# Kernel tuning notes

Measured on AMD Instinct MI355X. Metric: run time of the kernel, lower is better.

The kernel has to match this reference:

```python
import jax, jax.numpy as jnp
import numpy as np

B, T, C, H, O = 64, 256, 2048, 512, 11
THRESHOLD = 1.0
LEAK = 0.003
OUTPUT_LEAK = LEAK * 0.5


def setup_inputs() -> dict:
    key = jax.random.key(0)
    k1, k2, k3, k4 = jax.random.split(key, 4)
    x = jax.random.normal(k1, (B, T, C), dtype=jnp.float32)
    # xavier_uniform(gain=0.1) for fc1: bound = 0.1*sqrt(6/(C+H))
    b1 = 0.1 * np.sqrt(6.0 / (C + H))
    w1 = jax.random.uniform(k2, (H, C), jnp.float32, -b1, b1)
    # orthogonal(gain=0.1) for fc_rec -> approximate with small gaussian scaled like orthogonal rows
    w_rec = 0.1 * jnp.linalg.qr(jax.random.normal(k3, (H, H), jnp.float32))[0]
    b2 = 0.3 * np.sqrt(6.0 / (H + O))
    w2 = jax.random.uniform(k4, (O, H), jnp.float32, -b2, b2)
    return {"x": x, "w1": w1, "w_rec": w_rec, "w2": w2}


def reference(x, w1, w_rec, w2):
    batch, t_steps, _ = x.shape
    n_hidden = w1.shape[0]
    n_output = w2.shape[0]
    dt = x.dtype

    def step(carry, x_t):
        v1, spk1, v2, out_sum = carry
        # input + recurrent current: [B,H]
        i1 = x_t @ w1.T + spk1 @ w_rec.T
        # subtractive LIF: leak, threshold, subtractive reset
        v1 = v1 + i1 - LEAK
        spk = (v1 >= THRESHOLD).astype(dt)
        v1 = v1 - spk * THRESHOLD
        # non-spiking output accumulator neuron: [B,O]
        i2 = spk @ w2.T
        v2 = jnp.maximum(v2 + i2 - OUTPUT_LEAK, 0.0)
        out_sum = out_sum + v2
        return (v1, spk, v2, out_sum), None

    init = (
        jnp.zeros((batch, n_hidden), dt),
        jnp.zeros((batch, n_hidden), dt),
        jnp.zeros((batch, n_output), dt),
        jnp.zeros((batch, n_output), dt),
    )
    (_, _, _, out_sum), _ = jax.lax.scan(step, init, jnp.swapaxes(x, 0, 1))
    return out_sum / t_steps
```

## Files before the change

kernel.cpp:

```cpp
#include <hip/hip_runtime.h>
#include <cstddef>

#define B_ 64
#define T_ 256
#define C_ 2048
#define H_ 512
#define O_ 11
#define THRESH 1.0f
#define LEAK_ 0.003f
#define OLEAK_ 0.0015f

typedef float v2f __attribute__((ext_vector_type(2)));

__global__ __launch_bounds__(256) void transpose_wrec(const float* __restrict__ w,
                                                      float* __restrict__ wt) {
    __shared__ float tile[32][33];
    int tx = threadIdx.x, ty = threadIdx.y;
    int x = blockIdx.x * 32 + tx;
    int y = blockIdx.y * 32 + ty;
#pragma unroll
    for (int i = 0; i < 32; i += 8)
        tile[ty + i][tx] = w[(size_t)(y + i) * H_ + x];
    __syncthreads();
    int x2 = blockIdx.y * 32 + tx;
    int y2 = blockIdx.x * 32 + ty;
#pragma unroll
    for (int i = 0; i < 32; i += 8)
        wt[(size_t)(y2 + i) * H_ + x2] = tile[tx][ty + i];
}

#define BM 256
#define BN 128
#define BK 16

template <int S>
__global__ __launch_bounds__(256, 2) void gemm_ff(const float* __restrict__ A,
                                                  const float* __restrict__ Bw,
                                                  float* __restrict__ Pout) {
    const int K = C_;
    const int N = H_;
    const int kLen  = C_ / S;
    const int kBase = blockIdx.z * kLen;

    __shared__ float As[BK][BM + 4];
    __shared__ float Bs[BK][BN + 4];

    const int t  = threadIdx.x;
    const int tx = t & 15;
    const int ty = t >> 4;
    const int lr = t >> 2;
    const int lc = (t & 3) * 4;

    const float* Aptr = A  + (size_t)(blockIdx.y * BM + lr) * K + kBase + lc;
    const float* Bptr = Bw + (size_t)(blockIdx.x * BN + lr) * K + kBase + lc;

    v2f acc[16][4];
#pragma unroll
    for (int i = 0; i < 16; ++i)
#pragma unroll
        for (int j = 0; j < 4; ++j) acc[i][j] = (v2f){0.f, 0.f};

    for (int k0 = 0; k0 < kLen; k0 += BK) {
        float4 a0 = *(const float4*)(Aptr);
        float4 a1 = *(const float4*)(Aptr + (size_t)64  * K);
        float4 a2 = *(const float4*)(Aptr + (size_t)128 * K);
        float4 a3 = *(const float4*)(Aptr + (size_t)192 * K);
        float4 b0 = *(const float4*)(Bptr);
        float4 b1 = *(const float4*)(Bptr + (size_t)64 * K);
        Aptr += BK; Bptr += BK;

        __syncthreads();
        As[lc + 0][lr]       = a0.x; As[lc + 1][lr]       = a0.y;
        As[lc + 2][lr]       = a0.z; As[lc + 3][lr]       = a0.w;
        As[lc + 0][lr + 64]  = a1.x; As[lc + 1][lr + 64]  = a1.y;
        As[lc + 2][lr + 64]  = a1.z; As[lc + 3][lr + 64]  = a1.w;
        As[lc + 0][lr + 128] = a2.x; As[lc + 1][lr + 128] = a2.y;
        As[lc + 2][lr + 128] = a2.z; As[lc + 3][lr + 128] = a2.w;
        As[lc + 0][lr + 192] = a3.x; As[lc + 1][lr + 192] = a3.y;
        As[lc + 2][lr + 192] = a3.z; As[lc + 3][lr + 192] = a3.w;
        Bs[lc + 0][lr]       = b0.x; Bs[lc + 1][lr]       = b0.y;
        Bs[lc + 2][lr]       = b0.z; Bs[lc + 3][lr]       = b0.w;
        Bs[lc + 0][lr + 64]  = b1.x; Bs[lc + 1][lr + 64]  = b1.y;
        Bs[lc + 2][lr + 64]  = b1.z; Bs[lc + 3][lr + 64]  = b1.w;
        __syncthreads();

#pragma unroll
        for (int k = 0; k < BK; ++k) {
            float4 af0 = *(const float4*)&As[k][ty * 8];
            float4 af1 = *(const float4*)&As[k][ty * 8 + 4];
            float4 af2 = *(const float4*)&As[k][128 + ty * 8];
            float4 af3 = *(const float4*)&As[k][128 + ty * 8 + 4];
            float4 blo = *(const float4*)&Bs[k][tx * 4];
            float4 bhi = *(const float4*)&Bs[k][64 + tx * 4];
            v2f b0v = {blo.x, blo.y}, b1v = {blo.z, blo.w};
            v2f b2v = {bhi.x, bhi.y}, b3v = {bhi.z, bhi.w};
            float av[16] = {af0.x, af0.y, af0.z, af0.w, af1.x, af1.y, af1.z, af1.w,
                            af2.x, af2.y, af2.z, af2.w, af3.x, af3.y, af3.z, af3.w};
#pragma unroll
            for (int i = 0; i < 16; ++i) {
                v2f ai = {av[i], av[i]};
                acc[i][0] += ai * b0v;
                acc[i][1] += ai * b1v;
                acc[i][2] += ai * b2v;
                acc[i][3] += ai * b3v;
            }
        }
    }

    float* P = Pout + (size_t)blockIdx.z * ((size_t)B_ * T_ * H_);
#pragma unroll
    for (int i = 0; i < 16; ++i) {
        int row = blockIdx.y * BM + (i < 8 ? ty * 8 + i : 128 + ty * 8 + (i - 8));
        float* Cp = P + (size_t)row * N + blockIdx.x * BN;
        float4 c0 = {acc[i][0].x, acc[i][0].y, acc[i][1].x, acc[i][1].y};
        float4 c1 = {acc[i][2].x, acc[i][2].y, acc[i][3].x, acc[i][3].y};
        *(float4*)(Cp + tx * 4)      = c0;
        *(float4*)(Cp + 64 + tx * 4) = c1;
    }
}

template <int S>
__global__ __launch_bounds__(256) void reduce_parts(float* __restrict__ P) {
    const size_t n = (size_t)B_ * T_ * H_;
    size_t i = ((size_t)blockIdx.x * 256 + threadIdx.x) * 4;
    if (i >= n) return;
    float4 a = *(float4*)(P + i);
#pragma unroll
    for (int s = 1; s < S; ++s) {
        float4 bq = *(const float4*)(P + (size_t)s * n + i);
        a.x += bq.x; a.y += bq.y; a.z += bq.z; a.w += bq.w;
    }
    *(float4*)(P + i) = a;
}

__global__ __launch_bounds__(64) void snn_rec(const float* __restrict__ I1,
                                              const float* __restrict__ wrT,
                                              const float* __restrict__ w2,
                                              float* __restrict__ out) {
    const int b = blockIdx.x;
    const int L = threadIdx.x;

    const float* i1p = I1 + (size_t)b * T_ * H_ + L;
    const float* wrL = wrT + L;
    const float* w2L = w2 + (size_t)(L < O_ ? L : 0) * H_;

    float v1[8], pf[8];
    unsigned long long masks[8];
#pragma unroll
    for (int r = 0; r < 8; ++r) { v1[r] = 0.f; masks[r] = 0ull; pf[r] = i1p[r * 64]; }
    float v2 = 0.f, osum = 0.f;

    for (int t = 0; t < T_; ++t) {
        float acc[8];
#pragma unroll
        for (int r = 0; r < 8; ++r) acc[r] = pf[r] - LEAK_;

        const float* nx = i1p + (size_t)((t + 1 < T_) ? t + 1 : t) * H_;
#pragma unroll
        for (int r = 0; r < 8; ++r) pf[r] = nx[r * 64];

#pragma unroll
        for (int r2 = 0; r2 < 8; ++r2) {
            unsigned long long m = masks[r2];
            while (m) {
                int j = (r2 << 6) + __builtin_ctzll(m);
                m &= (m - 1);
                const float* wj = wrL + (size_t)j * H_;
#pragma unroll
                for (int r = 0; r < 8; ++r) acc[r] += wj[r * 64];
            }
        }

#pragma unroll
        for (int r = 0; r < 8; ++r) v1[r] += acc[r];
#pragma unroll
        for (int r = 0; r < 8; ++r) {
            masks[r] = __ballot(v1[r] >= THRESH);
            if (v1[r] >= THRESH) v1[r] -= THRESH;
        }

        float s = 0.f;
        if (L < O_) {
#pragma unroll
            for (int r2 = 0; r2 < 8; ++r2) {
                unsigned long long m = masks[r2];
                while (m) {
                    int j = (r2 << 6) + __builtin_ctzll(m);
                    m &= (m - 1);
                    s += w2L[j];
                }
            }
        }
        v2 = v2 + s - OLEAK_;
        v2 = v2 > 0.f ? v2 : 0.f;
        osum += v2;
    }
    if (L < O_) out[b * O_ + L] = osum * (1.0f / (float)T_);
}

extern "C" void kernel_launch(void* const* d_in, const int* in_sizes, int n_in,
                              void* d_out, int out_size, void* d_ws, size_t ws_size,
                              hipStream_t stream) {
    const float* x     = (const float*)d_in[0];
    const float* w1    = (const float*)d_in[1];
    const float* w_rec = (const float*)d_in[2];
    const float* w2    = (const float*)d_in[3];
    float* out = (float*)d_out;

    const size_t PART = (size_t)B_ * T_ * H_ * sizeof(float);
    const size_t WRT  = (size_t)H_ * H_ * sizeof(float);

    int S = 1;
    if (ws_size >= 4 * PART + WRT) S = 4;
    else if (ws_size >= 2 * PART + WRT) S = 2;

    float* P   = (float*)d_ws;
    float* wrT = (float*)((char*)d_ws + (size_t)S * PART);

    transpose_wrec<<<dim3(H_ / 32, H_ / 32), dim3(32, 8), 0, stream>>>(w_rec, wrT);

    dim3 ggrid(H_ / BN, (B_ * T_) / BM, S);
    const int rblocks = (int)(((size_t)B_ * T_ * H_ / 4 + 255) / 256);
    switch (S) {
        case 4:
            gemm_ff<4><<<ggrid, dim3(256), 0, stream>>>(x, w1, P);
            reduce_parts<4><<<dim3(rblocks), dim3(256), 0, stream>>>(P);
            break;
        case 2:
            gemm_ff<2><<<ggrid, dim3(256), 0, stream>>>(x, w1, P);
            reduce_parts<2><<<dim3(rblocks), dim3(256), 0, stream>>>(P);
            break;
        default:
            gemm_ff<1><<<ggrid, dim3(256), 0, stream>>>(x, w1, P);
            break;
    }
    snn_rec<<<dim3(B_), dim3(64), 0, stream>>>(P, wrT, w2, out);
}
```

Baseline: 777.5 us.

## Prefetch GEMM tiles in registers and restructure recurrent spike loop with batched gathers

The feedforward GEMM now uses 128x128 tiles with 128 threads and loads the next K-slice into registers while the current tile is computed, overlapping global loads with FMA work. The recurrent kernel builds a compact spike index list in shared memory each step and gathers recurrent weight rows in batches of eight, so loads can be issued in parallel instead of serially per spike. The output-neuron accumulation moves out of the time loop: spike masks are stored in shared memory and the output currents are computed in parallel after the loop. The trade-offs are more registers in the GEMM, more shared memory, and some redundant clamped loads in the gather.

Result: slower. 894.4 us (+15.0%).

```diff
diff --git a/kernel.cpp b/kernel.cpp
--- a/kernel.cpp
+++ b/kernel.cpp
@@ -29,12 +29,12 @@
         wt[(size_t)(y2 + i) * H_ + x2] = tile[tx][ty + i];
 }
 
-#define BM 256
+#define BM 128
 #define BN 128
 #define BK 16
 
 template <int S>
-__global__ __launch_bounds__(256, 2) void gemm_ff(const float* __restrict__ A,
+__global__ __launch_bounds__(128, 2) void gemm_ff(const float* __restrict__ A,
                                                   const float* __restrict__ Bw,
                                                   float* __restrict__ Pout) {
     const int K = C_;
@@ -51,8 +51,16 @@
     const int lr = t >> 2;
     const int lc = (t & 3) * 4;
 
-    const float* Aptr = A  + (size_t)(blockIdx.y * BM + lr) * K + kBase + lc;
-    const float* Bptr = Bw + (size_t)(blockIdx.x * BN + lr) * K + kBase + lc;
+    const float* Ap = A  + (size_t)(blockIdx.y * BM + lr) * K + kBase + lc;
+    const float* Bp = Bw + (size_t)(blockIdx.x * BN + lr) * K + kBase + lc;
+
+    float4 ar[4], br[4];
+#pragma unroll
+    for (int q = 0; q < 4; ++q) {
+        ar[q] = *(const float4*)(Ap + (size_t)(q * 32) * K);
+        br[q] = *(const float4*)(Bp + (size_t)(q * 32) * K);
+    }
+    Ap += BK; Bp += BK;
 
     v2f acc[16][4];
 #pragma unroll
@@ -60,42 +68,39 @@
 #pragma unroll
         for (int j = 0; j < 4; ++j) acc[i][j] = (v2f){0.f, 0.f};
 
-    for (int k0 = 0; k0 < kLen; k0 += BK) {
-        float4 a0 = *(const float4*)(Aptr);
-        float4 a1 = *(const float4*)(Aptr + (size_t)64  * K);
-        float4 a2 = *(const float4*)(Aptr + (size_t)128 * K);
-        float4 a3 = *(const float4*)(Aptr + (size_t)192 * K);
-        float4 b0 = *(const float4*)(Bptr);
-        float4 b1 = *(const float4*)(Bptr + (size_t)64 * K);
-        Aptr += BK; Bptr += BK;
-
+    const int nT = kLen / BK;
+    for (int kt = 0; kt < nT; ++kt) {
         __syncthreads();
-        As[lc + 0][lr]       = a0.x; As[lc + 1][lr]       = a0.y;
-        As[lc + 2][lr]       = a0.z; As[lc + 3][lr]       = a0.w;
-        As[lc + 0][lr + 64]  = a1.x; As[lc + 1][lr + 64]  = a1.y;
-        As[lc + 2][lr + 64]  = a1.z; As[lc + 3][lr + 64]  = a1.w;
-        As[lc + 0][lr + 128] = a2.x; As[lc + 1][lr + 128] = a2.y;
-        As[lc + 2][lr + 128] = a2.z; As[lc + 3][lr + 128] = a2.w;
-        As[lc + 0][lr + 192] = a3.x; As[lc + 1][lr + 192] = a3.y;
-        As[lc + 2][lr + 192] = a3.z; As[lc + 3][lr + 192] = a3.w;
-        Bs[lc + 0][lr]       = b0.x; Bs[lc + 1][lr]       = b0.y;
-        Bs[lc + 2][lr]       = b0.z; Bs[lc + 3][lr]       = b0.w;
-        Bs[lc + 0][lr + 64]  = b1.x; Bs[lc + 1][lr + 64]  = b1.y;
-        Bs[lc + 2][lr + 64]  = b1.z; Bs[lc + 3][lr + 64]  = b1.w;
+#pragma unroll
+        for (int q = 0; q < 4; ++q) {
+            As[lc + 0][lr + q * 32] = ar[q].x; As[lc + 1][lr + q * 32] = ar[q].y;
+            As[lc + 2][lr + q * 32] = ar[q].z; As[lc + 3][lr + q * 32] = ar[q].w;
+            Bs[lc + 0][lr + q * 32] = br[q].x; Bs[lc + 1][lr + q * 32] = br[q].y;
+            Bs[lc + 2][lr + q * 32] = br[q].z; Bs[lc + 3][lr + q * 32] = br[q].w;
+        }
         __syncthreads();
 
+        if (kt + 1 < nT) {
+#pragma unroll
+            for (int q = 0; q < 4; ++q) {
+                ar[q] = *(const float4*)(Ap + (size_t)(q * 32) * K);
+                br[q] = *(const float4*)(Bp + (size_t)(q * 32) * K);
+            }
+            Ap += BK; Bp += BK;
+        }
+
 #pragma unroll
         for (int k = 0; k < BK; ++k) {
-            float4 af0 = *(const float4*)&As[k][ty * 8];
-            float4 af1 = *(const float4*)&As[k][ty * 8 + 4];
-            float4 af2 = *(const float4*)&As[k][128 + ty * 8];
-            float4 af3 = *(const float4*)&As[k][128 + ty * 8 + 4];
-            float4 blo = *(const float4*)&Bs[k][tx * 4];
-            float4 bhi = *(const float4*)&Bs[k][64 + tx * 4];
-            v2f b0v = {blo.x, blo.y}, b1v = {blo.z, blo.w};
-            v2f b2v = {bhi.x, bhi.y}, b3v = {bhi.z, bhi.w};
-            float av[16] = {af0.x, af0.y, af0.z, af0.w, af1.x, af1.y, af1.z, af1.w,
-                            af2.x, af2.y, af2.z, af2.w, af3.x, af3.y, af3.z, af3.w};
+            float4 a0 = *(const float4*)&As[k][ty * 8];
+            float4 a1 = *(const float4*)&As[k][ty * 8 + 4];
+            float4 a2 = *(const float4*)&As[k][64 + ty * 8];
+            float4 a3 = *(const float4*)&As[k][64 + ty * 8 + 4];
+            float4 bq0 = *(const float4*)&Bs[k][tx * 4];
+            float4 bq1 = *(const float4*)&Bs[k][64 + tx * 4];
+            v2f b0v = {bq0.x, bq0.y}, b1v = {bq0.z, bq0.w};
+            v2f b2v = {bq1.x, bq1.y}, b3v = {bq1.z, bq1.w};
+            float av[16] = {a0.x, a0.y, a0.z, a0.w, a1.x, a1.y, a1.z, a1.w,
+                            a2.x, a2.y, a2.z, a2.w, a3.x, a3.y, a3.z, a3.w};
 #pragma unroll
             for (int i = 0; i < 16; ++i) {
                 v2f ai = {av[i], av[i]};
@@ -110,7 +115,7 @@
     float* P = Pout + (size_t)blockIdx.z * ((size_t)B_ * T_ * H_);
 #pragma unroll
     for (int i = 0; i < 16; ++i) {
-        int row = blockIdx.y * BM + (i < 8 ? ty * 8 + i : 128 + ty * 8 + (i - 8));
+        int row = blockIdx.y * BM + (i < 8 ? ty * 8 + i : 64 + ty * 8 + (i - 8));
         float* Cp = P + (size_t)row * N + blockIdx.x * BN;
         float4 c0 = {acc[i][0].x, acc[i][0].y, acc[i][1].x, acc[i][1].y};
         float4 c1 = {acc[i][2].x, acc[i][2].y, acc[i][3].x, acc[i][3].y};
@@ -140,62 +145,124 @@
     const int b = blockIdx.x;
     const int L = threadIdx.x;
 
+    __shared__ int                smask_lo[T_ * 8];
+    __shared__ int                smask_hi[T_ * 8];
+    __shared__ int                slist[2][H_];
+    __shared__ float              w2t[H_ * 12];
+    __shared__ float              i2s[T_ * 12];
+
     const float* i1p = I1 + (size_t)b * T_ * H_ + L;
-    const float* wrL = wrT + L;
-    const float* w2L = w2 + (size_t)(L < O_ ? L : 0) * H_;
 
     float v1[8], pf[8];
-    unsigned long long masks[8];
-#pragma unroll
-    for (int r = 0; r < 8; ++r) { v1[r] = 0.f; masks[r] = 0ull; pf[r] = i1p[r * 64]; }
-    float v2 = 0.f, osum = 0.f;
+#pragma unroll
+    for (int r = 0; r < 8; ++r) { v1[r] = 0.f; pf[r] = i1p[r * 64]; }
+
+    const unsigned long long below = (L == 0) ? 0ull : ((~0ull) >> (64 - L));
+    int pcnt = 0;
 
     for (int t = 0; t < T_; ++t) {
-        float acc[8];
-#pragma unroll
-        for (int r = 0; r < 8; ++r) acc[r] = pf[r] - LEAK_;
+        const int pb = t & 1;
+        const int prev = pb ^ 1;
+
+        float racc[8];
+#pragma unroll
+        for (int r = 0; r < 8; ++r) racc[r] = pf[r] - LEAK_;
+
+        for (int base = 0; base < pcnt; base += 8) {
+            int jj[8];
+#pragma unroll
+            for (int s = 0; s < 8; ++s) {
+                int ii = base + s;
+                if (ii > pcnt - 1) ii = pcnt - 1;
+                jj[s] = slist[prev][ii];
+            }
+            float vv[8][8];
+#pragma unroll
+            for (int s = 0; s < 8; ++s) {
+                const float* wj = wrT + (size_t)jj[s] * H_ + L;
+#pragma unroll
+                for (int r = 0; r < 8; ++r) vv[s][r] = wj[r * 64];
+            }
+#pragma unroll
+            for (int s = 0; s < 8; ++s) {
+                if (base + s < pcnt) {
+#pragma unroll
+                    for (int r = 0; r < 8; ++r) racc[r] += vv[s][r];
+                }
+            }
+        }
+
+        unsigned long long mk[8];
+#pragma unroll
+        for (int r = 0; r < 8; ++r) {
+            v1[r] += racc[r];
+            bool sp = (v1[r] >= THRESH);
+            mk[r] = __ballot(sp);
+            if (sp) v1[r] -= THRESH;
+        }
+
+        if (L == 0) {
+#pragma unroll
+            for (int r = 0; r < 8; ++r) {
+                smask_lo[t * 8 + r] = (int)(mk[r] & 0xffffffffull);
+                smask_hi[t * 8 + r] = (int)(mk[r] >> 32);
+            }
+        }
+
+        int cb = 0;
+#pragma unroll
+        for (int r = 0; r < 8; ++r) {
+            int pos = (int)__popcll(mk[r] & below);
+            if ((mk[r] >> L) & 1ull) slist[pb][cb + pos] = (r << 6) + L;
+            cb += (int)__popcll(mk[r]);
+        }
+        pcnt = cb;
 
         const float* nx = i1p + (size_t)((t + 1 < T_) ? t + 1 : t) * H_;
 #pragma unroll
         for (int r = 0; r < 8; ++r) pf[r] = nx[r * 64];
-
-#pragma unroll
-        for (int r2 = 0; r2 < 8; ++r2) {
-            unsigned long long m = masks[r2];
+    }
+
+    __syncthreads();
+
+    for (int j = L; j < H_; j += 64) {
+#pragma unroll
+        for (int o = 0; o < O_; ++o) w2t[j * 12 + o] = w2[o * H_ + j];
+    }
+    __syncthreads();
+
+    for (int tt = L; tt < T_; tt += 64) {
+        float s0 = 0.f, s1 = 0.f, s2 = 0.f, s3 = 0.f, s4 = 0.f, s5 = 0.f,
+              s6 = 0.f, s7 = 0.f, s8 = 0.f, s9 = 0.f, s10 = 0.f;
+#pragma unroll
+        for (int r = 0; r < 8; ++r) {
+            unsigned long long m =
+                ((unsigned long long)(unsigned)smask_lo[tt * 8 + r]) |
+                (((unsigned long long)(unsigned)smask_hi[tt * 8 + r]) << 32);
             while (m) {
-                int j = (r2 << 6) + __builtin_ctzll(m);
-                m &= (m - 1);
-                const float* wj = wrL + (size_t)j * H_;
-#pragma unroll
-                for (int r = 0; r < 8; ++r) acc[r] += wj[r * 64];
-            }
-        }
-
-#pragma unroll
-        for (int r = 0; r < 8; ++r) v1[r] += acc[r];
-#pragma unroll
-        for (int r = 0; r < 8; ++r) {
-            masks[r] = __ballot(v1[r] >= THRESH);
-            if (v1[r] >= THRESH) v1[r] -= THRESH;
-        }
-
-        float s = 0.f;
-        if (L < O_) {
-#pragma unroll
-            for (int r2 = 0; r2 < 8; ++r2) {
-                unsigned long long m = masks[r2];
-                while (m) {
-                    int j = (r2 << 6) + __builtin_ctzll(m);
-                    m &= (m - 1);
-                    s += w2L[j];
-                }
-            }
-        }
-        v2 = v2 + s - OLEAK_;
-        v2 = v2 > 0.f ? v2 : 0.f;
-        osum += v2;
-    }
-    if (L < O_) out[b * O_ + L] = osum * (1.0f / (float)T_);
+                int j = (r << 6) + __builtin_ctzll(m);
+                m &= m - 1;
+                const float* wp = &w2t[j * 12];
+                s0 += wp[0]; s1 += wp[1]; s2 += wp[2]; s3 += wp[3];
+                s4 += wp[4]; s5 += wp[5]; s6 += wp[6]; s7 += wp[7];
+                s8 += wp[8]; s9 += wp[9]; s10 += wp[10];
+            }
+        }
+        float* ip = &i2s[tt * 12];
+        ip[0] = s0; ip[1] = s1; ip[2] = s2; ip[3] = s3; ip[4] = s4;
+        ip[5] = s5; ip[6] = s6; ip[7] = s7; ip[8] = s8; ip[9] = s9; ip[10] = s10;
+    }
+    __syncthreads();
+
+    if (L < O_) {
+        float v2 = 0.f, osum = 0.f;
+        for (int t = 0; t < T_; ++t) {
+            v2 = v2 + i2s[t * 12 + L] - OLEAK_;
+            v2 = v2 > 0.f ? v2 : 0.f;
+            osum += v2;
+        }
+        out[b * O_ + L] = osum * (1.0f / (float)T_);
+    }
 }
 
 extern "C" void kernel_launch(void* const* d_in, const int* in_sizes, int n_in,
@@ -223,15 +290,15 @@
     const int rblocks = (int)(((size_t)B_ * T_ * H_ / 4 + 255) / 256);
     switch (S) {
         case 4:
-            gemm_ff<4><<<ggrid, dim3(256), 0, stream>>>(x, w1, P);
+            gemm_ff<4><<<ggrid, dim3(128), 0, stream>>>(x, w1, P);
             reduce_parts<4><<<dim3(rblocks), dim3(256), 0, stream>>>(P);
             break;
         case 2:
-            gemm_ff<2><<<ggrid, dim3(256), 0, stream>>>(x, w1, P);
+            gemm_ff<2><<<ggrid, dim3(128), 0, stream>>>(x, w1, P);
             reduce_parts<2><<<dim3(rblocks), dim3(256), 0, stream>>>(P);
             break;
         default:
-            gemm_ff<1><<<ggrid, dim3(256), 0, stream>>>(x, w1, P);
+            gemm_ff<1><<<ggrid, dim3(128), 0, stream>>>(x, w1, P);
             break;
     }
     snn_rec<<<dim3(B_), dim3(64), 0, stream>>>(P, wrT, w2, out);
```

## Fuse split-K reduction into recurrence, compact spike lists, retile GEMM with prefetch

Applied to the files above, without the earlier changes.

Drops the separate reduce_parts kernel and sums the split-K partial planes inside the recurrent kernel as it streams each timestep. The recurrence now gives each lane 8 contiguous neurons, builds a compacted spike index list in shared memory, and gathers recurrent weights in unrolled float4 batches of eight. The output-neuron accumulation is moved out of the serial time loop into a parallel pass over stored spike masks. The GEMM is retiled to 128x128 with a swizzled 1D block index and register prefetch of the next K tile. The trade-off is more global reads per timestep in the serial kernel, S partial planes instead of one, and more shared memory per block.

Result: slower. 931.0 us (+19.7%).

```diff
diff --git a/kernel.cpp b/kernel.cpp
--- a/kernel.cpp
+++ b/kernel.cpp
@@ -12,6 +12,10 @@
 
 typedef float v2f __attribute__((ext_vector_type(2)));
 
+__device__ __forceinline__ float4 f4add(float4 a, float4 b) {
+    return make_float4(a.x + b.x, a.y + b.y, a.z + b.z, a.w + b.w);
+}
+
 __global__ __launch_bounds__(256) void transpose_wrec(const float* __restrict__ w,
                                                       float* __restrict__ wt) {
     __shared__ float tile[32][33];
@@ -29,18 +33,24 @@
         wt[(size_t)(y2 + i) * H_ + x2] = tile[tx][ty + i];
 }
 
-#define BM 256
+#define BM 128
 #define BN 128
 #define BK 16
 
 template <int S>
-__global__ __launch_bounds__(256, 2) void gemm_ff(const float* __restrict__ A,
-                                                  const float* __restrict__ Bw,
-                                                  float* __restrict__ Pout) {
+__global__ __launch_bounds__(256) void gemm_ff(const float* __restrict__ A,
+                                               const float* __restrict__ Bw,
+                                               float* __restrict__ Pout) {
     const int K = C_;
     const int N = H_;
-    const int kLen  = C_ / S;
-    const int kBase = blockIdx.z * kLen;
+    const int kLen = C_ / S;
+
+    int lid = blockIdx.x;
+    int z   = lid >> 9;
+    int rem = lid & 511;
+    int by  = (rem >> 5) * 8 + (rem & 7);
+    int bx  = (rem >> 3) & 3;
+    const int kBase = z * kLen;
 
     __shared__ float As[BK][BM + 4];
     __shared__ float Bs[BK][BN + 4];
@@ -51,53 +61,53 @@
     const int lr = t >> 2;
     const int lc = (t & 3) * 4;
 
-    const float* Aptr = A  + (size_t)(blockIdx.y * BM + lr) * K + kBase + lc;
-    const float* Bptr = Bw + (size_t)(blockIdx.x * BN + lr) * K + kBase + lc;
-
-    v2f acc[16][4];
-#pragma unroll
-    for (int i = 0; i < 16; ++i)
+    const float* Ap = A  + (size_t)(by * BM + lr) * K + kBase + lc;
+    const float* Bp = Bw + (size_t)(bx * BN + lr) * K + kBase + lc;
+
+    float4 pa0 = *(const float4*)(Ap);
+    float4 pa1 = *(const float4*)(Ap + (size_t)64 * K);
+    float4 pb0 = *(const float4*)(Bp);
+    float4 pb1 = *(const float4*)(Bp + (size_t)64 * K);
+    Ap += BK; Bp += BK;
+
+    v2f acc[8][4];
+#pragma unroll
+    for (int i = 0; i < 8; ++i)
 #pragma unroll
         for (int j = 0; j < 4; ++j) acc[i][j] = (v2f){0.f, 0.f};
 
-    for (int k0 = 0; k0 < kLen; k0 += BK) {
-        float4 a0 = *(const float4*)(Aptr);
-        float4 a1 = *(const float4*)(Aptr + (size_t)64  * K);
-        float4 a2 = *(const float4*)(Aptr + (size_t)128 * K);
-        float4 a3 = *(const float4*)(Aptr + (size_t)192 * K);
-        float4 b0 = *(const float4*)(Bptr);
-        float4 b1 = *(const float4*)(Bptr + (size_t)64 * K);
-        Aptr += BK; Bptr += BK;
-
+    const int nT = kLen / BK;
+    for (int kt = 0; kt < nT; ++kt) {
         __syncthreads();
-        As[lc + 0][lr]       = a0.x; As[lc + 1][lr]       = a0.y;
-        As[lc + 2][lr]       = a0.z; As[lc + 3][lr]       = a0.w;
-        As[lc + 0][lr + 64]  = a1.x; As[lc + 1][lr + 64]  = a1.y;
-        As[lc + 2][lr + 64]  = a1.z; As[lc + 3][lr + 64]  = a1.w;
-        As[lc + 0][lr + 128] = a2.x; As[lc + 1][lr + 128] = a2.y;
-        As[lc + 2][lr + 128] = a2.z; As[lc + 3][lr + 128] = a2.w;
-        As[lc + 0][lr + 192] = a3.x; As[lc + 1][lr + 192] = a3.y;
-        As[lc + 2][lr + 192] = a3.z; As[lc + 3][lr + 192] = a3.w;
-        Bs[lc + 0][lr]       = b0.x; Bs[lc + 1][lr]       = b0.y;
-        Bs[lc + 2][lr]       = b0.z; Bs[lc + 3][lr]       = b0.w;
-        Bs[lc + 0][lr + 64]  = b1.x; Bs[lc + 1][lr + 64]  = b1.y;
-        Bs[lc + 2][lr + 64]  = b1.z; Bs[lc + 3][lr + 64]  = b1.w;
+        As[lc + 0][lr] = pa0.x; As[lc + 1][lr] = pa0.y;
+        As[lc + 2][lr] = pa0.z; As[lc + 3][lr] = pa0.w;
+        As[lc + 0][lr + 64] = pa1.x; As[lc + 1][lr + 64] = pa1.y;
+        As[lc + 2][lr + 64] = pa1.z; As[lc + 3][lr + 64] = pa1.w;
+        Bs[lc + 0][lr] = pb0.x; Bs[lc + 1][lr] = pb0.y;
+        Bs[lc + 2][lr] = pb0.z; Bs[lc + 3][lr] = pb0.w;
+        Bs[lc + 0][lr + 64] = pb1.x; Bs[lc + 1][lr + 64] = pb1.y;
+        Bs[lc + 2][lr + 64] = pb1.z; Bs[lc + 3][lr + 64] = pb1.w;
         __syncthreads();
 
+        if (kt + 1 < nT) {
+            pa0 = *(const float4*)(Ap);
+            pa1 = *(const float4*)(Ap + (size_t)64 * K);
+            pb0 = *(const float4*)(Bp);
+            pb1 = *(const float4*)(Bp + (size_t)64 * K);
+            Ap += BK; Bp += BK;
+        }
+
 #pragma unroll
         for (int k = 0; k < BK; ++k) {
-            float4 af0 = *(const float4*)&As[k][ty * 8];
-            float4 af1 = *(const float4*)&As[k][ty * 8 + 4];
-            float4 af2 = *(const float4*)&As[k][128 + ty * 8];
-            float4 af3 = *(const float4*)&As[k][128 + ty * 8 + 4];
+            float4 alo = *(const float4*)&As[k][ty * 4];
+            float4 ahi = *(const float4*)&As[k][64 + ty * 4];
             float4 blo = *(const float4*)&Bs[k][tx * 4];
             float4 bhi = *(const float4*)&Bs[k][64 + tx * 4];
             v2f b0v = {blo.x, blo.y}, b1v = {blo.z, blo.w};
             v2f b2v = {bhi.x, bhi.y}, b3v = {bhi.z, bhi.w};
-            float av[16] = {af0.x, af0.y, af0.z, af0.w, af1.x, af1.y, af1.z, af1.w,
-                            af2.x, af2.y, af2.z, af2.w, af3.x, af3.y, af3.z, af3.w};
-#pragma unroll
-            for (int i = 0; i < 16; ++i) {
+            float av[8] = {alo.x, alo.y, alo.z, alo.w, ahi.x, ahi.y, ahi.z, ahi.w};
+#pragma unroll
+            for (int i = 0; i < 8; ++i) {
                 v2f ai = {av[i], av[i]};
                 acc[i][0] += ai * b0v;
                 acc[i][1] += ai * b1v;
@@ -107,11 +117,11 @@
         }
     }
 
-    float* P = Pout + (size_t)blockIdx.z * ((size_t)B_ * T_ * H_);
-#pragma unroll
-    for (int i = 0; i < 16; ++i) {
-        int row = blockIdx.y * BM + (i < 8 ? ty * 8 + i : 128 + ty * 8 + (i - 8));
-        float* Cp = P + (size_t)row * N + blockIdx.x * BN;
+    float* P = Pout + (size_t)z * ((size_t)B_ * T_ * H_);
+#pragma unroll
+    for (int i = 0; i < 8; ++i) {
+        int row = by * BM + (i < 4 ? ty * 4 + i : 64 + ty * 4 + (i - 4));
+        float* Cp = P + (size_t)row * N + bx * BN;
         float4 c0 = {acc[i][0].x, acc[i][0].y, acc[i][1].x, acc[i][1].y};
         float4 c1 = {acc[i][2].x, acc[i][2].y, acc[i][3].x, acc[i][3].y};
         *(float4*)(Cp + tx * 4)      = c0;
@@ -120,82 +130,186 @@
 }
 
 template <int S>
-__global__ __launch_bounds__(256) void reduce_parts(float* __restrict__ P) {
-    const size_t n = (size_t)B_ * T_ * H_;
-    size_t i = ((size_t)blockIdx.x * 256 + threadIdx.x) * 4;
-    if (i >= n) return;
-    float4 a = *(float4*)(P + i);
-#pragma unroll
-    for (int s = 1; s < S; ++s) {
-        float4 bq = *(const float4*)(P + (size_t)s * n + i);
-        a.x += bq.x; a.y += bq.y; a.z += bq.z; a.w += bq.w;
-    }
-    *(float4*)(P + i) = a;
-}
-
-__global__ __launch_bounds__(64) void snn_rec(const float* __restrict__ I1,
+__global__ __launch_bounds__(64) void snn_rec(const float* __restrict__ P,
                                               const float* __restrict__ wrT,
                                               const float* __restrict__ w2,
                                               float* __restrict__ out) {
     const int b = blockIdx.x;
     const int L = threadIdx.x;
-
-    const float* i1p = I1 + (size_t)b * T_ * H_ + L;
-    const float* wrL = wrT + L;
-    const float* w2L = w2 + (size_t)(L < O_ ? L : 0) * H_;
-
-    float v1[8], pf[8];
-    unsigned long long masks[8];
-#pragma unroll
-    for (int r = 0; r < 8; ++r) { v1[r] = 0.f; masks[r] = 0ull; pf[r] = i1p[r * 64]; }
-    float v2 = 0.f, osum = 0.f;
-
-    for (int t = 0; t < T_; ++t) {
-        float acc[8];
-#pragma unroll
-        for (int r = 0; r < 8; ++r) acc[r] = pf[r] - LEAK_;
-
-        const float* nx = i1p + (size_t)((t + 1 < T_) ? t + 1 : t) * H_;
-#pragma unroll
-        for (int r = 0; r < 8; ++r) pf[r] = nx[r * 64];
-
-#pragma unroll
-        for (int r2 = 0; r2 < 8; ++r2) {
-            unsigned long long m = masks[r2];
+    const size_t PARTF = (size_t)B_ * T_ * H_;
+
+    __shared__ int   smask_lo[T_ * 8];
+    __shared__ int   smask_hi[T_ * 8];
+    __shared__ int   slist[H_];
+    __shared__ float w2t[H_ * 12];
+    __shared__ float i2s[T_ * 12];
+
+    const float* rowb = P + (size_t)b * T_ * H_ + 8 * L;
+    const float* wrL  = wrT + 8 * L;
+
+    float v1[8];
+#pragma unroll
+    for (int r = 0; r < 8; ++r) v1[r] = 0.f;
+    int pcnt = 0;
+
+    const unsigned long long below = (L == 0) ? 0ull : ((~0ull) >> (64 - L));
+
+    float4 pA[S][2], pB[S][2];
+#pragma unroll
+    for (int s = 0; s < S; ++s) {
+        pA[s][0] = *(const float4*)(rowb + s * PARTF);
+        pA[s][1] = *(const float4*)(rowb + s * PARTF + 4);
+        pB[s][0] = *(const float4*)(rowb + s * PARTF + H_);
+        pB[s][1] = *(const float4*)(rowb + s * PARTF + H_ + 4);
+    }
+
+#define SNN_STEP(tcur, PC)                                                     \
+    {                                                                          \
+        const int t = (tcur);                                                  \
+        float4 rc0 = make_float4(-LEAK_, -LEAK_, -LEAK_, -LEAK_);              \
+        float4 rc1 = rc0;                                                      \
+        _Pragma("unroll")                                                      \
+        for (int s = 0; s < S; ++s) {                                          \
+            rc0 = f4add(rc0, PC[s][0]);                                        \
+            rc1 = f4add(rc1, PC[s][1]);                                        \
+        }                                                                      \
+        if (pcnt > 0) {                                                        \
+            const int lim = pcnt - 1;                                          \
+            for (int base = 0; base < pcnt; base += 8) {                       \
+                int i1q = base + 1 > lim ? lim : base + 1;                     \
+                int i2q = base + 2 > lim ? lim : base + 2;                     \
+                int i3q = base + 3 > lim ? lim : base + 3;                     \
+                int i4q = base + 4 > lim ? lim : base + 4;                     \
+                int i5q = base + 5 > lim ? lim : base + 5;                     \
+                int i6q = base + 6 > lim ? lim : base + 6;                     \
+                int i7q = base + 7 > lim ? lim : base + 7;                     \
+                int j0 = slist[base];                                          \
+                int j1 = slist[i1q]; int j2 = slist[i2q];                      \
+                int j3 = slist[i3q]; int j4 = slist[i4q];                      \
+                int j5 = slist[i5q]; int j6 = slist[i6q];                      \
+                int j7 = slist[i7q];                                           \
+                const float* q0 = wrL + (size_t)j0 * H_;                       \
+                const float* q1 = wrL + (size_t)j1 * H_;                       \
+                const float* q2 = wrL + (size_t)j2 * H_;                       \
+                const float* q3 = wrL + (size_t)j3 * H_;                       \
+                const float* q4 = wrL + (size_t)j4 * H_;                       \
+                const float* q5 = wrL + (size_t)j5 * H_;                       \
+                const float* q6 = wrL + (size_t)j6 * H_;                       \
+                const float* q7 = wrL + (size_t)j7 * H_;                       \
+                float4 g0a = *(const float4*)q0, g0b = *(const float4*)(q0 + 4); \
+                float4 g1a = *(const float4*)q1, g1b = *(const float4*)(q1 + 4); \
+                float4 g2a = *(const float4*)q2, g2b = *(const float4*)(q2 + 4); \
+                float4 g3a = *(const float4*)q3, g3b = *(const float4*)(q3 + 4); \
+                float4 g4a = *(const float4*)q4, g4b = *(const float4*)(q4 + 4); \
+                float4 g5a = *(const float4*)q5, g5b = *(const float4*)(q5 + 4); \
+                float4 g6a = *(const float4*)q6, g6b = *(const float4*)(q6 + 4); \
+                float4 g7a = *(const float4*)q7, g7b = *(const float4*)(q7 + 4); \
+                rc0 = f4add(rc0, g0a); rc1 = f4add(rc1, g0b);                  \
+                if (base + 1 < pcnt) { rc0 = f4add(rc0, g1a); rc1 = f4add(rc1, g1b); } \
+                if (base + 2 < pcnt) { rc0 = f4add(rc0, g2a); rc1 = f4add(rc1, g2b); } \
+                if (base + 3 < pcnt) { rc0 = f4add(rc0, g3a); rc1 = f4add(rc1, g3b); } \
+                if (base + 4 < pcnt) { rc0 = f4add(rc0, g4a); rc1 = f4add(rc1, g4b); } \
+                if (base + 5 < pcnt) { rc0 = f4add(rc0, g5a); rc1 = f4add(rc1, g5b); } \
+                if (base + 6 < pcnt) { rc0 = f4add(rc0, g6a); rc1 = f4add(rc1, g6b); } \
+                if (base + 7 < pcnt) { rc0 = f4add(rc0, g7a); rc1 = f4add(rc1, g7b); } \
+            }                                                                  \
+        }                                                                      \
+        float rcv[8] = {rc0.x, rc0.y, rc0.z, rc0.w, rc1.x, rc1.y, rc1.z, rc1.w}; \
+        unsigned long long mk0, mk1, mk2, mk3, mk4, mk5, mk6, mk7;             \
+        {                                                                      \
+            v1[0] += rcv[0]; bool sp = v1[0] >= THRESH; mk0 = __ballot(sp); if (sp) v1[0] -= THRESH; \
+        }                                                                      \
+        { v1[1] += rcv[1]; bool sp = v1[1] >= THRESH; mk1 = __ballot(sp); if (sp) v1[1] -= THRESH; } \
+        { v1[2] += rcv[2]; bool sp = v1[2] >= THRESH; mk2 = __ballot(sp); if (sp) v1[2] -= THRESH; } \
+        { v1[3] += rcv[3]; bool sp = v1[3] >= THRESH; mk3 = __ballot(sp); if (sp) v1[3] -= THRESH; } \
+        { v1[4] += rcv[4]; bool sp = v1[4] >= THRESH; mk4 = __ballot(sp); if (sp) v1[4] -= THRESH; } \
+        { v1[5] += rcv[5]; bool sp = v1[5] >= THRESH; mk5 = __ballot(sp); if (sp) v1[5] -= THRESH; } \
+        { v1[6] += rcv[6]; bool sp = v1[6] >= THRESH; mk6 = __ballot(sp); if (sp) v1[6] -= THRESH; } \
+        { v1[7] += rcv[7]; bool sp = v1[7] >= THRESH; mk7 = __ballot(sp); if (sp) v1[7] -= THRESH; } \
+        if (L == 0) {                                                          \
+            smask_lo[t * 8 + 0] = (int)(mk0 & 0xffffffffull); smask_hi[t * 8 + 0] = (int)(mk0 >> 32); \
+            smask_lo[t * 8 + 1] = (int)(mk1 & 0xffffffffull); smask_hi[t * 8 + 1] = (int)(mk1 >> 32); \
+            smask_lo[t * 8 + 2] = (int)(mk2 & 0xffffffffull); smask_hi[t * 8 + 2] = (int)(mk2 >> 32); \
+            smask_lo[t * 8 + 3] = (int)(mk3 & 0xffffffffull); smask_hi[t * 8 + 3] = (int)(mk3 >> 32); \
+            smask_lo[t * 8 + 4] = (int)(mk4 & 0xffffffffull); smask_hi[t * 8 + 4] = (int)(mk4 >> 32); \
+            smask_lo[t * 8 + 5] = (int)(mk5 & 0xffffffffull); smask_hi[t * 8 + 5] = (int)(mk5 >> 32); \
+            smask_lo[t * 8 + 6] = (int)(mk6 & 0xffffffffull); smask_hi[t * 8 + 6] = (int)(mk6 >> 32); \
+            smask_lo[t * 8 + 7] = (int)(mk7 & 0xffffffffull); smask_hi[t * 8 + 7] = (int)(mk7 >> 32); \
+        }                                                                      \
+        int Sl = (int)__popcll(mk0 & below) + (int)__popcll(mk1 & below) +     \
+                 (int)__popcll(mk2 & below) + (int)__popcll(mk3 & below) +     \
+                 (int)__popcll(mk4 & below) + (int)__popcll(mk5 & below) +     \
+                 (int)__popcll(mk6 & below) + (int)__popcll(mk7 & below);      \
+        int run = 0;                                                           \
+        if ((mk0 >> L) & 1ull) { slist[Sl + run] = 8 * L + 0; ++run; }         \
+        if ((mk1 >> L) & 1ull) { slist[Sl + run] = 8 * L + 1; ++run; }         \
+        if ((mk2 >> L) & 1ull) { slist[Sl + run] = 8 * L + 2; ++run; }         \
+        if ((mk3 >> L) & 1ull) { slist[Sl + run] = 8 * L + 3; ++run; }         \
+        if ((mk4 >> L) & 1ull) { slist[Sl + run] = 8 * L + 4; ++run; }         \
+        if ((mk5 >> L) & 1ull) { slist[Sl + run] = 8 * L + 5; ++run; }         \
+        if ((mk6 >> L) & 1ull) { slist[Sl + run] = 8 * L + 6; ++run; }         \
+        if ((mk7 >> L) & 1ull) { slist[Sl + run] = 8 * L + 7; ++run; }         \
+        pcnt = (int)__popcll(mk0) + (int)__popcll(mk1) + (int)__popcll(mk2) +  \
+               (int)__popcll(mk3) + (int)__popcll(mk4) + (int)__popcll(mk5) +  \
+               (int)__popcll(mk6) + (int)__popcll(mk7);                        \
+                       \
+        {                                                                      \
+            int nr = t + 2 < T_ ? t + 2 : T_ - 1;                              \
+            const float* nb2 = rowb + (size_t)nr * H_;                         \
+            _Pragma("unroll")                                                  \
+            for (int s = 0; s < S; ++s) {                                      \
+                PC[s][0] = *(const float4*)(nb2 + s * PARTF);                  \
+                PC[s][1] = *(const float4*)(nb2 + s * PARTF + 4);              \
+            }                                                                  \
+        }                                                                      \
+    }
+
+    for (int tt = 0; tt < T_; tt += 2) {
+        SNN_STEP(tt, pA)
+        SNN_STEP(tt + 1, pB)
+    }
+#undef SNN_STEP
+
+    __syncthreads();
+
+    for (int j = L; j < H_; j += 64) {
+#pragma unroll
+        for (int o = 0; o < O_; ++o) w2t[j * 12 + o] = w2[o * H_ + j];
+    }
+    __syncthreads();
+
+    for (int tt = L; tt < T_; tt += 64) {
+        float s0 = 0.f, s1 = 0.f, s2 = 0.f, s3 = 0.f, s4 = 0.f, s5 = 0.f,
+              s6 = 0.f, s7 = 0.f, s8 = 0.f, s9 = 0.f, s10 = 0.f;
+#pragma unroll
+        for (int r = 0; r < 8; ++r) {
+            unsigned long long m =
+                ((unsigned long long)(unsigned)smask_lo[tt * 8 + r]) |
+                (((unsigned long long)(unsigned)smask_hi[tt * 8 + r]) << 32);
             while (m) {
-                int j = (r2 << 6) + __builtin_ctzll(m);
-                m &= (m - 1);
-                const float* wj = wrL + (size_t)j * H_;
-#pragma unroll
-                for (int r = 0; r < 8; ++r) acc[r] += wj[r * 64];
+                int l = __builtin_ctzll(m);
+                m &= m - 1;
+                const float* wp = &w2t[(8 * l + r) * 12];
+                s0 += wp[0]; s1 += wp[1]; s2 += wp[2]; s3 += wp[3];
+                s4 += wp[4]; s5 += wp[5]; s6 += wp[6]; s7 += wp[7];
+                s8 += wp[8]; s9 += wp[9]; s10 += wp[10];
             }
         }
-
-#pragma unroll
-        for (int r = 0; r < 8; ++r) v1[r] += acc[r];
-#pragma unroll
-        for (int r = 0; r < 8; ++r) {
-            masks[r] = __ballot(v1[r] >= THRESH);
-            if (v1[r] >= THRESH) v1[r] -= THRESH;
+        float* ip = &i2s[tt * 12];
+        ip[0] = s0; ip[1] = s1; ip[2] = s2; ip[3] = s3; ip[4] = s4;
+        ip[5] = s5; ip[6] = s6; ip[7] = s7; ip[8] = s8; ip[9] = s9; ip[10] = s10;
+    }
+    __syncthreads();
+
+    if (L < O_) {
+        float v2 = 0.f, osum = 0.f;
+        for (int t = 0; t < T_; ++t) {
+            v2 = v2 + i2s[t * 12 + L] - OLEAK_;
+            v2 = v2 > 0.f ? v2 : 0.f;
+            osum += v2;
         }
-
-        float s = 0.f;
-        if (L < O_) {
-#pragma unroll
-            for (int r2 = 0; r2 < 8; ++r2) {
-                unsigned long long m = masks[r2];
-                while (m) {
-                    int j = (r2 << 6) + __builtin_ctzll(m);
-                    m &= (m - 1);
-                    s += w2L[j];
-                }
-            }
-        }
-        v2 = v2 + s - OLEAK_;
-        v2 = v2 > 0.f ? v2 : 0.f;
-        osum += v2;
-    }
-    if (L < O_) out[b * O_ + L] = osum * (1.0f / (float)T_);
+        out[b * O_ + L] = osum * (1.0f / (float)T_);
+    }
 }
 
 extern "C" void kernel_launch(void* const* d_in, const int* in_sizes, int n_in,
@@ -219,20 +333,18 @@
 
     transpose_wrec<<<dim3(H_ / 32, H_ / 32), dim3(32, 8), 0, stream>>>(w_rec, wrT);
 
-    dim3 ggrid(H_ / BN, (B_ * T_) / BM, S);
-    const int rblocks = (int)(((size_t)B_ * T_ * H_ / 4 + 255) / 256);
     switch (S) {
         case 4:
-            gemm_ff<4><<<ggrid, dim3(256), 0, stream>>>(x, w1, P);
-            reduce_parts<4><<<dim3(rblocks), dim3(256), 0, stream>>>(P);
+            gemm_ff<4><<<dim3(512 * 4), dim3(256), 0, stream>>>(x, w1, P);
+            snn_rec<4><<<dim3(B_), dim3(64), 0, stream>>>(P, wrT, w2, out);
             break;
         case 2:
-            gemm_ff<2><<<ggrid, dim3(256), 0, stream>>>(x, w1, P);
-            reduce_parts<2><<<dim3(rblocks), dim3(256), 0, stream>>>(P);
+            gemm_ff<2><<<dim3(512 * 2), dim3(256), 0, stream>>>(x, w1, P);
+            snn_rec<2><<<dim3(B_), dim3(64), 0, stream>>>(P, wrT, w2, out);
             break;
         default:
-            gemm_ff<1><<<ggrid, dim3(256), 0, stream>>>(x, w1, P);
+            gemm_ff<1><<<dim3(512), dim3(256), 0, stream>>>(x, w1, P);
+            snn_rec<1><<<dim3(B_), dim3(64), 0, stream>>>(P, wrT, w2, out);
             break;
     }
-    snn_rec<<<dim3(B_), dim3(64), 0, stream>>>(P, wrT, w2, out);
-}
+}
```
